# Optimization experiments

Hardware: AMD Instinct MI355X
Metric: run time of the kernel (lower is better)

Reference implementation:

```python
import jax, jax.numpy as jnp
import numpy as np

B, D, N, L, M = 32, 64, 128, 192, 32  # batch, channels, nodes, seq_len, modes
LH = L // 2 + 1  # rfft length = 97


def setup_inputs() -> dict:
    key = jax.random.key(0)
    k1, k2, k3 = jax.random.split(key, 3)
    scale = 1.0 / (D * D)  # 1/(in_channels*out_channels)
    q = jax.random.normal(k1, (B, D, N, L), dtype=jnp.float32)
    w_real = scale * jax.random.uniform(k2, (N, D, D, M), dtype=jnp.float32)
    w_imag = scale * jax.random.uniform(k3, (N, D, D, M), dtype=jnp.float32)
    return {"q": q, "w_real": w_real, "w_imag": w_imag}


def reference(q, w_real, w_imag):
    # mode_select_method='lowest' -> index = [0, 1, ..., M-1] (static)
    index = np.arange(M)
    x = jnp.transpose(q, (0, 2, 1, 3))            # [B, N, D, L]
    x_ft = jnp.fft.rfft(x, axis=-1)               # [B, N, D, LH] complex64
    w = (w_real + 1j * w_imag).astype(jnp.complex64)  # [N, D, D, M]
    sel = x_ft[..., index]                        # gather selected modes [B, N, D, M]
    # fused replacement of the per-mode einsum loop: one batched complex einsum
    out_sel = jnp.einsum('bnim,niom->bnom', sel, w)  # [B, N, D, M]
    out_ft = jnp.zeros((B, N, D, LH), dtype=jnp.complex64).at[..., :M].set(out_sel)
    out = jnp.fft.irfft(out_ft, n=L, axis=-1)     # [B, N, D, L] real
    return jnp.transpose(out, (0, 2, 1, 3))       # [B, D, N, L]
```

## Files before the change

### kernel.cpp

```cpp
#include <hip/hip_runtime.h>
#include <stdint.h>


typedef __attribute__((ext_vector_type(8))) short short8;
typedef __attribute__((ext_vector_type(4))) float f32x4;
typedef __attribute__((ext_vector_type(4))) unsigned short u16x4;

__device__ __forceinline__ unsigned short f2bf(float f) {
  union { float fv; uint32_t u; } v; v.fv = f;
  uint32_t u = v.u;
  u += 0x7fffu + ((u >> 16) & 1u);
  return (unsigned short)(u >> 16);
}

__device__ __forceinline__ f32x4 zero4() { f32x4 z; z[0]=0.f; z[1]=0.f; z[2]=0.f; z[3]=0.f; return z; }

#define TWO_PI_OVER_L (6.283185307179586f / 192.0f)

__global__ __launch_bounds__(512, 1)
void k1d_dft(const float* __restrict__ q, unsigned short* __restrict__ Xp) {
  extern __shared__ char smem[];
  unsigned short* qB0 = (unsigned short*)smem;
  unsigned short* qB1 = (unsigned short*)(smem + 51200);
  unsigned short* Fb  = (unsigned short*)(smem + 102400);
  unsigned short* XE  = (unsigned short*)(smem + 128000);
  const int t = threadIdx.x, lane = t & 63, w = t >> 6;
  const int l15 = lane & 15, g = lane >> 4;
  const int bid = blockIdx.x;
  const int ih = bid & 1, bq = (bid >> 1) & 7, nq = bid >> 4;
  const int b0 = bq * 4;

  int srow[12], sqd[12];
#pragma unroll
  for (int j = 0; j < 12; ++j) {
    int fq = (w * 12 + j) * 64 + lane;
    srow[j] = fq / 48;
    sqd[j] = fq - srow[j] * 48;
  }
  size_t qoff[12];
#pragma unroll
  for (int j = 0; j < 12; ++j) {
    int row = srow[j];
    int b = b0 + (row >> 5), i = ih * 32 + (row & 31);
    qoff[j] = ((size_t)((b * 64 + i) * 128)) * 192 + sqd[j] * 4;
  }
  float4 stg[12];
  {
    const int n0 = nq * 4;
#pragma unroll
    for (int j = 0; j < 12; ++j)
      stg[j] = *(const float4*)(q + qoff[j] + (size_t)n0 * 192);
  }

  for (int idx = t; idx < 64 * 192; idx += 512) {
    int cat = idx / 192, l = idx - cat * 192;
    int m = cat >> 1;
    int r = (m * l) % 192;
    float ang = (float)r * TWO_PI_OVER_L;
    float v = (cat & 1) ? -__sinf(ang) : __cosf(ang);
    Fb[cat * 200 + l] = f2bf(v);
  }

#pragma unroll
  for (int j = 0; j < 12; ++j) {
    u16x4 h; h[0] = f2bf(stg[j].x); h[1] = f2bf(stg[j].y);
    h[2] = f2bf(stg[j].z); h[3] = f2bf(stg[j].w);
    *(u16x4*)(qB0 + srow[j] * 200 + sqd[j] * 4) = h;
  }
  __syncthreads();

  for (int nn = 0; nn < 4; ++nn) {
    const int n = nq * 4 + nn;
    unsigned short* cur = (nn & 1) ? qB1 : qB0;
    unsigned short* nxt = (nn & 1) ? qB0 : qB1;

    if (nn < 3) {
#pragma unroll
      for (int j = 0; j < 12; ++j)
        stg[j] = *(const float4*)(q + qoff[j] + (size_t)(n + 1) * 192);
    }

    f32x4 acc[4];
#pragma unroll
    for (int a = 0; a < 4; ++a) acc[a] = zero4();
    const int row = w * 16 + l15;
#pragma unroll
    for (int kc = 0; kc < 6; ++kc) {
      short8 A = *(const short8*)(cur + row * 200 + kc * 32 + g * 8);
#pragma unroll
      for (int nt = 0; nt < 4; ++nt) {
        short8 Bf = *(const short8*)(Fb + (nt * 16 + l15) * 200 + kc * 32 + g * 8);
        acc[nt] = __builtin_amdgcn_mfma_f32_16x16x32_bf16(A, Bf, acc[nt], 0, 0, 0);
      }
    }

    if (nn < 3) {
#pragma unroll
      for (int j = 0; j < 12; ++j) {
        u16x4 h; h[0] = f2bf(stg[j].x); h[1] = f2bf(stg[j].y);
        h[2] = f2bf(stg[j].z); h[3] = f2bf(stg[j].w);
        *(u16x4*)(nxt + srow[j] * 200 + sqd[j] * 4) = h;
      }
    }
    __syncthreads();

    const int b_loc = w >> 1, i_base = (w & 1) * 16 + g * 4;
#pragma unroll
    for (int nt = 0; nt < 4; ++nt) {
      int cat = nt * 16 + l15;
      f32x4 v = acc[nt];
#pragma unroll
      for (int r = 0; r < 4; ++r)
        XE[cat * 132 + b_loc * 32 + i_base + r] = f2bf(v[r]);
    }
    __syncthreads();

#pragma unroll
    for (int cc2 = 0; cc2 < 2; ++cc2) {
      int ch = cc2 * 512 + t;
      int m = ch >> 5, c = (ch >> 4) & 1, g2 = (ch >> 2) & 3, dl = ch & 3;
      short8 v = *(const short8*)(XE + (2 * m + c) * 132 + dl * 32 + g2 * 8);
      int lanep = g2 * 16 + (b0 & 15) + dl;
      int off = n * 131072 + ((((m * 2 + c) * 2 + ih) * 2 + (b0 >> 4)) * 64 + lanep) * 8;
      *(short8*)(Xp + off) = v;
    }
  }
}

#define M_OSTRIDE 18
#define M_ISTRIDE 290
#define M_CSTRIDE 18560
__global__ __launch_bounds__(512, 4)
void k2m_mix(const float* __restrict__ wr, const float* __restrict__ wi,
             const unsigned short* __restrict__ Xp, unsigned short* __restrict__ Yp) {
  extern __shared__ char smem[];
  unsigned short* T = (unsigned short*)smem;
  const int t = threadIdx.x, lane = t & 63, w = t >> 6;
  const int mh = blockIdx.x & 1, oq = (blockIdx.x >> 1) & 3, n = blockIdx.x >> 3;
  const int ol = lane & 15, il0 = (lane >> 4) * 8;

#pragma unroll
  for (int j = 0; j < 16; ++j) {
    int f = j * 512 + t;
    int mg = f & 3, o = (f >> 2) & 15, i = (f >> 6) & 63, c = (f >> 12) & 1;
    const float* src = (c ? wi : wr) + ((n * 64 + i) * 64 + oq * 16 + o) * 32 + mh * 16 + mg * 4;
    float4 v = *(const float4*)src;
    u16x4 h; h[0] = f2bf(v.x); h[1] = f2bf(v.y); h[2] = f2bf(v.z); h[3] = f2bf(v.w);
    *(u16x4*)(T + c * M_CSTRIDE + i * M_ISTRIDE + o * M_OSTRIDE + mg * 4) = h;
  }
  __syncthreads();

  unsigned short* yblk = Yp + (n * 4 + oq) * 32768;

#pragma unroll
  for (int mm = 0; mm < 2; ++mm) {
    int m_loc = w * 2 + mm;
    int m = mh * 16 + m_loc;
    f32x4 acc[2][2];
#pragma unroll
    for (int a = 0; a < 2; ++a)
#pragma unroll
      for (int b2 = 0; b2 < 2; ++b2) acc[a][b2] = zero4();

#pragma unroll
    for (int ic = 0; ic < 2; ++ic) {
      const unsigned short* xb = Xp + n * 131072 + m * 4096 + ic * 1024 + lane * 8;
      short8 Ar0 = *(const short8*)(xb);
      short8 Ar1 = *(const short8*)(xb + 512);
      short8 Ai0 = *(const short8*)(xb + 2048);
      short8 Ai1 = *(const short8*)(xb + 2048 + 512);

      const unsigned short* tb = T + (ic * 32 + il0) * M_ISTRIDE + ol * M_OSTRIDE + m_loc;
      short8 Br, Bi, nBi;
#pragma unroll
      for (int e = 0; e < 8; ++e) {
        Br[e] = (short)tb[e * M_ISTRIDE];
        Bi[e] = (short)tb[M_CSTRIDE + e * M_ISTRIDE];
        nBi[e] = Bi[e] ^ (short)0x8000;
      }

      acc[0][0] = __builtin_amdgcn_mfma_f32_16x16x32_bf16(Ar0, Br,  acc[0][0], 0, 0, 0);
      acc[0][0] = __builtin_amdgcn_mfma_f32_16x16x32_bf16(Ai0, nBi, acc[0][0], 0, 0, 0);
      acc[0][1] = __builtin_amdgcn_mfma_f32_16x16x32_bf16(Ar1, Br,  acc[0][1], 0, 0, 0);
      acc[0][1] = __builtin_amdgcn_mfma_f32_16x16x32_bf16(Ai1, nBi, acc[0][1], 0, 0, 0);
      acc[1][0] = __builtin_amdgcn_mfma_f32_16x16x32_bf16(Ar0, Bi,  acc[1][0], 0, 0, 0);
      acc[1][0] = __builtin_amdgcn_mfma_f32_16x16x32_bf16(Ai0, Br,  acc[1][0], 0, 0, 0);
      acc[1][1] = __builtin_amdgcn_mfma_f32_16x16x32_bf16(Ar1, Bi,  acc[1][1], 0, 0, 0);
      acc[1][1] = __builtin_amdgcn_mfma_f32_16x16x32_bf16(Ai1, Br,  acc[1][1], 0, 0, 0);
    }

    const int g = lane >> 4;
#pragma unroll
    for (int Mt = 0; Mt < 2; ++Mt)
#pragma unroll
      for (int r = 0; r < 4; ++r) {
        int b = Mt * 16 + g * 4 + r;
        unsigned short* yb = yblk + b * 1024 + (2 * m) * 16 + ol;
        yb[0]  = f2bf(acc[0][Mt][r]);
        yb[16] = f2bf(acc[1][Mt][r]);
      }
  }
}

__global__ __launch_bounds__(256, 4)
void k3_idft(const unsigned short* __restrict__ Yp, float* __restrict__ out) {
  extern __shared__ char smem[];
  unsigned short* Yl = (unsigned short*)smem;
  float* ol = (float*)(smem + 8448);
  const int t = threadIdx.x, lane = t & 63, w = t >> 6;
  const int n = blockIdx.x & 127, b = blockIdx.x >> 7;

  const unsigned short* ysrc = Yp + (n * 4 * 32 + b) * 1024;
#pragma unroll
  for (int j = 0; j < 2; ++j) {
    int f = j * 256 + t;
    int og = f & 1, cat = (f >> 1) & 63, oq = f >> 7;
    short8 v = *(const short8*)(ysrc + oq * 32768 + cat * 16 + og * 8);
    unsigned int* d = (unsigned int*)(Yl + cat * 66 + oq * 16 + og * 8);
    union { short8 s; unsigned int u[4]; } uu; uu.s = v;
    d[0] = uu.u[0]; d[1] = uu.u[1]; d[2] = uu.u[2]; d[3] = uu.u[3];
  }

  short8 Af[3][2];
#pragma unroll
  for (int jm = 0; jm < 3; ++jm) {
    int Mt = w + 4 * jm;
    int lt = Mt * 16 + (lane & 15);
#pragma unroll
    for (int kc = 0; kc < 2; ++kc) {
#pragma unroll
      for (int e = 0; e < 8; ++e) {
        int cat = kc * 32 + (lane >> 4) * 8 + e;
        int m = cat >> 1;
        int r = (m * lt) % 192;
        float ang = (float)r * TWO_PI_OVER_L;
        float coef = (m == 0) ? (1.0f / 192.0f) : (2.0f / 192.0f);
        float v = ((cat & 1) ? -__sinf(ang) : __cosf(ang)) * coef;
        Af[jm][kc][e] = (short)f2bf(v);
      }
    }
  }
  __syncthreads();

  f32x4 acc[3][4];
#pragma unroll
  for (int a = 0; a < 3; ++a)
#pragma unroll
    for (int bq = 0; bq < 4; ++bq) acc[a][bq] = zero4();

#pragma unroll
  for (int kc = 0; kc < 2; ++kc) {
    short8 Bf[4];
#pragma unroll
    for (int nt = 0; nt < 4; ++nt)
#pragma unroll
      for (int e = 0; e < 8; ++e) {
        int cat = kc * 32 + (lane >> 4) * 8 + e;
        Bf[nt][e] = (short)Yl[cat * 66 + nt * 16 + (lane & 15)];
      }
#pragma unroll
    for (int jm = 0; jm < 3; ++jm)
#pragma unroll
      for (int nt = 0; nt < 4; ++nt)
        acc[jm][nt] = __builtin_amdgcn_mfma_f32_16x16x32_bf16(Af[jm][kc], Bf[nt], acc[jm][nt], 0, 0, 0);
  }

#pragma unroll
  for (int jm = 0; jm < 3; ++jm) {
    int Mt = w + 4 * jm;
    int l0 = Mt * 16 + (lane >> 4) * 4;
#pragma unroll
    for (int nt = 0; nt < 4; ++nt) {
      int o = nt * 16 + (lane & 15);
      int lp = l0 ^ ((o & 7) << 2);
      *(f32x4*)(ol + o * 192 + lp) = acc[jm][nt];
    }
  }
  __syncthreads();

  float* dst = out + (b * 64 * 128 + n) * 192;
#pragma unroll
  for (int j = 0; j < 12; ++j) {
    int f = j * 256 + t;
    int o = f / 48, g2 = f - o * 48;
    int lp = g2 * 4;
    int l = lp ^ ((o & 7) << 2);
    f32x4 v = *(const f32x4*)(ol + o * 192 + lp);
    *(f32x4*)(dst + o * (128 * 192) + l) = v;
  }
}

extern "C" void kernel_launch(void* const* d_in, const int* in_sizes, int n_in,
                              void* d_out, int out_size, void* d_ws, size_t ws_size,
                              hipStream_t stream) {
  const float* q  = (const float*)d_in[0];
  const float* wr = (const float*)d_in[1];
  const float* wi = (const float*)d_in[2];
  float* out = (float*)d_out;

  unsigned short* Xp = (unsigned short*)d_ws;
  unsigned short* Yp = Xp + 16777216;

  hipFuncSetAttribute((const void*)k1d_dft, hipFuncAttributeMaxDynamicSharedMemorySize, 144896);
  hipFuncSetAttribute((const void*)k2m_mix, hipFuncAttributeMaxDynamicSharedMemorySize, 74240);
  hipFuncSetAttribute((const void*)k3_idft, hipFuncAttributeMaxDynamicSharedMemorySize, 57600);

  k1d_dft<<<dim3(512), dim3(512), 144896, stream>>>(q, Xp);
  k2m_mix<<<dim3(1024), dim3(512), 74240, stream>>>(wr, wi, Xp, Yp);
  k3_idft<<<dim3(4096), dim3(256), 57600, stream>>>(Yp, out);
}
```

Baseline: 179.4 us.

## Merge mode halves into one mix block with prefetched weight loads

The mixing kernel now processes both halves of the mode range in a single block per (node, output quarter), using two shared-memory weight tiles. The second half's weights are loaded into registers while the first half's MFMA work runs, overlapping global weight fetches with compute. The cost is half as many blocks, double the shared memory per block, occupancy limited to one block per CU, and 64 float4 registers held per thread for the prefetch.

```diff
diff --git a/kernel.cpp b/kernel.cpp
--- a/kernel.cpp
+++ b/kernel.cpp
@@ -127,35 +127,18 @@
   }
 }
 
-#define M_OSTRIDE 18
-#define M_ISTRIDE 290
-#define M_CSTRIDE 18560
-__global__ __launch_bounds__(512, 4)
-void k2m_mix(const float* __restrict__ wr, const float* __restrict__ wi,
-             const unsigned short* __restrict__ Xp, unsigned short* __restrict__ Yp) {
-  extern __shared__ char smem[];
-  unsigned short* T = (unsigned short*)smem;
-  const int t = threadIdx.x, lane = t & 63, w = t >> 6;
-  const int mh = blockIdx.x & 1, oq = (blockIdx.x >> 1) & 3, n = blockIdx.x >> 3;
-  const int ol = lane & 15, il0 = (lane >> 4) * 8;
-
-#pragma unroll
-  for (int j = 0; j < 16; ++j) {
-    int f = j * 512 + t;
-    int mg = f & 3, o = (f >> 2) & 15, i = (f >> 6) & 63, c = (f >> 12) & 1;
-    const float* src = (c ? wi : wr) + ((n * 64 + i) * 64 + oq * 16 + o) * 32 + mh * 16 + mg * 4;
-    float4 v = *(const float4*)src;
-    u16x4 h; h[0] = f2bf(v.x); h[1] = f2bf(v.y); h[2] = f2bf(v.z); h[3] = f2bf(v.w);
-    *(u16x4*)(T + c * M_CSTRIDE + i * M_ISTRIDE + o * M_OSTRIDE + mg * 4) = h;
-  }
-  __syncthreads();
-
-  unsigned short* yblk = Yp + (n * 4 + oq) * 32768;
-
+#define P_OSTRIDE 18
+#define P_ISTRIDE 290
+#define P_CSTRIDE 18560
+
+__device__ __forceinline__ void k2p_chunk(const unsigned short* __restrict__ T,
+    int mbase, int n, const unsigned short* __restrict__ Xp,
+    unsigned short* __restrict__ yblk, int lane, int w) {
+  const int ol = lane & 15, il0 = (lane >> 4) * 8, g = lane >> 4;
 #pragma unroll
   for (int mm = 0; mm < 2; ++mm) {
     int m_loc = w * 2 + mm;
-    int m = mh * 16 + m_loc;
+    int m = mbase + m_loc;
     f32x4 acc[2][2];
 #pragma unroll
     for (int a = 0; a < 2; ++a)
@@ -168,14 +151,14 @@
       short8 Ar0 = *(const short8*)(xb);
       short8 Ar1 = *(const short8*)(xb + 512);
       short8 Ai0 = *(const short8*)(xb + 2048);
-      short8 Ai1 = *(const short8*)(xb + 2048 + 512);
-
-      const unsigned short* tb = T + (ic * 32 + il0) * M_ISTRIDE + ol * M_OSTRIDE + m_loc;
+      short8 Ai1 = *(const short8*)(xb + 2560);
+
+      const unsigned short* tb = T + (ic * 32 + il0) * P_ISTRIDE + ol * P_OSTRIDE + m_loc;
       short8 Br, Bi, nBi;
 #pragma unroll
       for (int e = 0; e < 8; ++e) {
-        Br[e] = (short)tb[e * M_ISTRIDE];
-        Bi[e] = (short)tb[M_CSTRIDE + e * M_ISTRIDE];
+        Br[e] = (short)tb[e * P_ISTRIDE];
+        Bi[e] = (short)tb[P_CSTRIDE + e * P_ISTRIDE];
         nBi[e] = Bi[e] ^ (short)0x8000;
       }
 
@@ -189,7 +172,6 @@
       acc[1][1] = __builtin_amdgcn_mfma_f32_16x16x32_bf16(Ai1, Br,  acc[1][1], 0, 0, 0);
     }
 
-    const int g = lane >> 4;
 #pragma unroll
     for (int Mt = 0; Mt < 2; ++Mt)
 #pragma unroll
@@ -200,6 +182,56 @@
         yb[16] = f2bf(acc[1][Mt][r]);
       }
   }
+}
+
+__global__ __launch_bounds__(512, 1)
+void k2p_mix(const float* __restrict__ wr, const float* __restrict__ wi,
+             const unsigned short* __restrict__ Xp, unsigned short* __restrict__ Yp) {
+  extern __shared__ char smem[];
+  unsigned short* T0 = (unsigned short*)smem;
+  unsigned short* T1 = (unsigned short*)(smem + 74240);
+  const int t = threadIdx.x, lane = t & 63, w = t >> 6;
+  const int n = blockIdx.x >> 2, oq = blockIdx.x & 3;
+
+  float4 s[16];
+#pragma unroll
+  for (int j = 0; j < 16; ++j) {
+    int f = j * 512 + t;
+    int mg = f & 3, o = (f >> 2) & 15, i = (f >> 6) & 63, c = (f >> 12) & 1;
+    s[j] = *(const float4*)((c ? wi : wr) +
+            ((n * 64 + i) * 64 + oq * 16 + o) * 32 + mg * 4);
+  }
+#pragma unroll
+  for (int j = 0; j < 16; ++j) {
+    int f = j * 512 + t;
+    int mg = f & 3, o = (f >> 2) & 15, i = (f >> 6) & 63, c = (f >> 12) & 1;
+    u16x4 h; h[0] = f2bf(s[j].x); h[1] = f2bf(s[j].y); h[2] = f2bf(s[j].z); h[3] = f2bf(s[j].w);
+    *(u16x4*)(T0 + c * P_CSTRIDE + i * P_ISTRIDE + o * P_OSTRIDE + mg * 4) = h;
+  }
+  __syncthreads();
+
+  unsigned short* yblk = Yp + (n * 4 + oq) * 32768;
+
+#pragma unroll
+  for (int j = 0; j < 16; ++j) {
+    int f = j * 512 + t;
+    int mg = f & 3, o = (f >> 2) & 15, i = (f >> 6) & 63, c = (f >> 12) & 1;
+    s[j] = *(const float4*)((c ? wi : wr) +
+            ((n * 64 + i) * 64 + oq * 16 + o) * 32 + 16 + mg * 4);
+  }
+
+  k2p_chunk(T0, 0, n, Xp, yblk, lane, w);
+
+#pragma unroll
+  for (int j = 0; j < 16; ++j) {
+    int f = j * 512 + t;
+    int mg = f & 3, o = (f >> 2) & 15, i = (f >> 6) & 63, c = (f >> 12) & 1;
+    u16x4 h; h[0] = f2bf(s[j].x); h[1] = f2bf(s[j].y); h[2] = f2bf(s[j].z); h[3] = f2bf(s[j].w);
+    *(u16x4*)(T1 + c * P_CSTRIDE + i * P_ISTRIDE + o * P_OSTRIDE + mg * 4) = h;
+  }
+  __syncthreads();
+
+  k2p_chunk(T1, 16, n, Xp, yblk, lane, w);
 }
 
 __global__ __launch_bounds__(256, 4)
@@ -302,10 +334,10 @@
   unsigned short* Yp = Xp + 16777216;
 
   hipFuncSetAttribute((const void*)k1d_dft, hipFuncAttributeMaxDynamicSharedMemorySize, 144896);
-  hipFuncSetAttribute((const void*)k2m_mix, hipFuncAttributeMaxDynamicSharedMemorySize, 74240);
+  hipFuncSetAttribute((const void*)k2p_mix, hipFuncAttributeMaxDynamicSharedMemorySize, 148480);
   hipFuncSetAttribute((const void*)k3_idft, hipFuncAttributeMaxDynamicSharedMemorySize, 57600);
 
   k1d_dft<<<dim3(512), dim3(512), 144896, stream>>>(q, Xp);
-  k2m_mix<<<dim3(1024), dim3(512), 74240, stream>>>(wr, wi, Xp, Yp);
+  k2p_mix<<<dim3(512), dim3(512), 148480, stream>>>(wr, wi, Xp, Yp);
   k3_idft<<<dim3(4096), dim3(256), 57600, stream>>>(Yp, out);
 }
```

Result: slower. 187.2 us (+4.4%).
